# Performance work log

Measured on AMD Instinct MI355X. Metric: run time of the kernel, lower is better.

Reference implementation:

```python
import jax, jax.numpy as jnp
import numpy as np

DIM = 768
NUM_HEADS = 12
HEAD_DIM = DIM // NUM_HEADS
SCALE = HEAD_DIM ** -0.5


def setup_inputs() -> dict:
    key = jax.random.key(0)
    k1, k2, k3, k4 = jax.random.split(key, 4)
    B, N = 4, 2048
    x = jax.random.normal(k1, (B, N, DIM), dtype=jnp.float32)
    w_qkv = jax.random.normal(k2, (DIM, 3 * DIM), dtype=jnp.float32) * (DIM ** -0.5)
    w_proj = jax.random.normal(k3, (DIM, DIM), dtype=jnp.float32) * (DIM ** -0.5)
    b_proj = jax.random.normal(k4, (DIM,), dtype=jnp.float32) * 0.02
    return {"x": x, "w_qkv": w_qkv, "w_proj": w_proj, "b_proj": b_proj}


def reference(x, w_qkv, w_proj, b_proj):
    B, N, C = x.shape
    H, Dh = NUM_HEADS, HEAD_DIM
    # qkv: [B, N, 3, H, Dh] -> q,k,v each [B, H, N, Dh]
    qkv = (x @ w_qkv).reshape(B, N, 3, H, Dh)
    q = qkv[:, :, 0].transpose(0, 2, 1, 3) * SCALE
    k = qkv[:, :, 1].transpose(0, 2, 1, 3)
    v = qkv[:, :, 2].transpose(0, 2, 1, 3)
    attn = jax.nn.softmax(jnp.einsum('bhnd,bhmd->bhnm', q, k), axis=-1)
    out = jnp.einsum('bhnm,bhmd->bhnd', attn, v)  # [B, H, N, Dh]
    out = out.transpose(0, 2, 1, 3).reshape(B, N, C)
    return out @ w_proj + b_proj
```

## Files before the change

kernel.cpp:

```cpp
#include <hip/hip_runtime.h>

typedef unsigned short u16;
typedef __bf16 bf16x8 __attribute__((ext_vector_type(8)));
typedef __bf16 bf16x4 __attribute__((ext_vector_type(4)));
typedef short s16x4 __attribute__((ext_vector_type(4)));
typedef float f32x4 __attribute__((ext_vector_type(4)));
typedef unsigned short u16x8 __attribute__((ext_vector_type(8)));
typedef unsigned short u16x4 __attribute__((ext_vector_type(4)));

__device__ __forceinline__ u16 f2bf(float x) {
  union { float f; unsigned u; } c; c.f = x;
  unsigned r = c.u + 0x7FFFu + ((c.u >> 16) & 1u);
  return (u16)(r >> 16);
}

__device__ __forceinline__ void glds16(const void* g, void* s) {
  __builtin_amdgcn_global_load_lds(
      (const __attribute__((address_space(1))) unsigned int*)g,
      (__attribute__((address_space(3))) unsigned int*)s, 16, 0, 0);
}

__global__ __launch_bounds__(256) void k_cast_x(const float* __restrict__ x,
                                                u16* __restrict__ o) {
  int i = blockIdx.x * 256 + threadIdx.x;
  const f32x4* xp = (const f32x4*)x + (size_t)i * 2;
  f32x4 a = xp[0], b = xp[1];
  u16x8 r;
  r[0] = f2bf(a[0]); r[1] = f2bf(a[1]); r[2] = f2bf(a[2]); r[3] = f2bf(a[3]);
  r[4] = f2bf(b[0]); r[5] = f2bf(b[1]); r[6] = f2bf(b[2]); r[7] = f2bf(b[3]);
  *((u16x8*)o + i) = r;
}

__global__ __launch_bounds__(256) void k_transpose_w(const float* __restrict__ src,
                                                     u16* __restrict__ dst,
                                                     int K, int Nn) {
  __shared__ float tile[64 * 68];
  int tid = threadIdx.x;
  int n0 = blockIdx.x * 64, k0 = blockIdx.y * 64;
  int rr = tid >> 4, cc = tid & 15;
#pragma unroll
  for (int r = 0; r < 4; ++r) {
    int k = r * 16 + rr;
    f32x4 v = *(const f32x4*)(src + (size_t)(k0 + k) * Nn + n0 + cc * 4);
    *(f32x4*)(tile + k * 68 + cc * 4) = v;
  }
  __syncthreads();
#pragma unroll
  for (int r = 0; r < 4; ++r) {
    int n = r * 16 + rr;
    u16x4 o;
#pragma unroll
    for (int j = 0; j < 4; ++j) o[j] = f2bf(tile[(cc * 4 + j) * 68 + n]);
    *(u16x4*)(dst + (size_t)(n0 + n) * K + k0 + cc * 4) = o;
  }
}

template <int N, bool PROJ>
__global__ __launch_bounds__(256) void k_gemm(const u16* __restrict__ A,
                                              const u16* __restrict__ Bt,
                                              u16* __restrict__ Co,
                                              float* __restrict__ Cf,
                                              const float* __restrict__ bias) {
  const int K = 768;
  __shared__ u16 lA[128 * 64];
  __shared__ u16 lB[128 * 64];
  const int tid = threadIdx.x;
  const int wave = tid >> 6, lane = tid & 63;
  const int lr = lane & 15, lq = lane >> 4;
  const int m0 = blockIdx.x * 128, n0 = blockIdx.y * 128;
  const int wr = (wave >> 1) * 64, wc = (wave & 1) * 64;
  f32x4 acc[4][4] = {};
  for (int k0 = 0; k0 < K; k0 += 64) {
#pragma unroll
    for (int r = 0; r < 4; ++r) {
      int ch = r * 256 + tid;
      int mm = ch >> 3, cs = ch & 7;
      int k8 = (cs ^ (mm & 7)) << 3;
      glds16(A + (size_t)(m0 + mm) * K + k0 + k8, lA + ch * 8);
      glds16(Bt + (size_t)(n0 + mm) * K + k0 + k8, lB + ch * 8);
    }
    __syncthreads();
#pragma unroll
    for (int ks = 0; ks < 2; ++ks) {
      bf16x8 af[4], bfr[4];
#pragma unroll
      for (int f = 0; f < 4; ++f) {
        int ma = wr + f * 16 + lr;
        af[f] = *(const bf16x8*)(lA + (ma * 8 + ((ks * 4 + lq) ^ (ma & 7))) * 8);
        int nb = wc + f * 16 + lr;
        bfr[f] = *(const bf16x8*)(lB + (nb * 8 + ((ks * 4 + lq) ^ (nb & 7))) * 8);
      }
#pragma unroll
      for (int fi = 0; fi < 4; ++fi)
#pragma unroll
        for (int fj = 0; fj < 4; ++fj)
          acc[fi][fj] = __builtin_amdgcn_mfma_f32_16x16x32_bf16(
              af[fi], bfr[fj], acc[fi][fj], 0, 0, 0);
    }
    __syncthreads();
  }
#pragma unroll
  for (int fi = 0; fi < 4; ++fi) {
#pragma unroll
    for (int fj = 0; fj < 4; ++fj) {
      int row = m0 + wr + fi * 16 + lq * 4;
      int col = n0 + wc + fj * 16 + lr;
      if constexpr (PROJ) {
        float bv = bias[col];
#pragma unroll
        for (int g = 0; g < 4; ++g)
          Cf[(size_t)(row + g) * N + col] = acc[fi][fj][g] + bv;
      } else {
        const float qs = 0.18033688011112042f;
        float s = (col < 768) ? qs : 1.0f;
#pragma unroll
        for (int g = 0; g < 4; ++g)
          Co[(size_t)(row + g) * N + col] = f2bf(acc[fi][fj][g] * s);
      }
    }
  }
}

__global__ __launch_bounds__(256) void k_vtrans(const u16* __restrict__ qkv,
                                                u16* __restrict__ vt) {
  __shared__ u16 tile[64 * 72];
  int tid = threadIdx.x;
  int n0 = blockIdx.x * 64;
  int bh = blockIdx.y;
  int b = bh / 12, h = bh % 12;
  const u16* src = qkv + (size_t)(b * 2048 + n0) * 2304 + 1536 + h * 64;
#pragma unroll
  for (int r = 0; r < 2; ++r) {
    int n = r * 32 + (tid >> 3), c8 = tid & 7;
    u16x8 v = *(const u16x8*)(src + (size_t)n * 2304 + c8 * 8);
    *(u16x8*)(tile + n * 72 + c8 * 8) = v;
  }
  __syncthreads();
  u16* dstb = vt + (size_t)bh * 64 * 2048 + n0;
#pragma unroll
  for (int r = 0; r < 2; ++r) {
    int d = r * 32 + (tid >> 3), n8 = tid & 7;
    u16x8 o;
#pragma unroll
    for (int j = 0; j < 8; ++j) o[j] = tile[(n8 * 8 + j) * 72 + d];
    *(u16x8*)(dstb + (size_t)d * 2048 + n8 * 8) = o;
  }
}

__global__ __launch_bounds__(256) void k_attn(const u16* __restrict__ qkv,
                                              const u16* __restrict__ vt,
                                              u16* __restrict__ aout) {
  const int SEQ = 2048, C3 = 2304;
  __shared__ u16 lK[128 * 64];
  __shared__ u16 lV[64 * 128];
  const int tid = threadIdx.x;
  const int wave = tid >> 6, lane = tid & 63;
  const int lr = lane & 15, lq = lane >> 4;
  const int n0 = blockIdx.x * 128;
  const int bh = blockIdx.y;
  const int b = bh / 12, h = bh % 12;
  const u16* qb = qkv + (size_t)b * SEQ * C3 + h * 64;
  const u16* kb = qb + 768;
  const u16* vb = vt + (size_t)bh * 64 * SEQ;

#pragma unroll
  for (int r = 0; r < 4; ++r) {
    int ch = r * 256 + tid;
    int mm = ch >> 3, cs = ch & 7;
    glds16(qb + (size_t)(n0 + mm) * C3 + ((cs ^ (mm & 7)) << 3), lK + ch * 8);
  }
  __syncthreads();
  bf16x8 qf[2][2];
#pragma unroll
  for (int rf = 0; rf < 2; ++rf) {
    int mq = wave * 32 + rf * 16 + lr;
#pragma unroll
    for (int ks = 0; ks < 2; ++ks)
      qf[rf][ks] = *(const bf16x8*)(lK + (mq * 8 + ((ks * 4 + lq) ^ (mq & 7))) * 8);
  }

  f32x4 O[2][4] = {};
  float lsum[2] = {0.f, 0.f};

  for (int j0 = 0; j0 < SEQ; j0 += 128) {
    __syncthreads();
#pragma unroll
    for (int r = 0; r < 4; ++r) {
      int ch = r * 256 + tid;
      int mm = ch >> 3, cs = ch & 7;
      glds16(kb + (size_t)(j0 + mm) * C3 + ((cs ^ (mm & 7)) << 3), lK + ch * 8);
      int dd = ch >> 4, ct = ch & 15;
      glds16(vb + (size_t)dd * SEQ + j0 + ((ct ^ (dd & 7)) << 3), lV + ch * 8);
    }
    __syncthreads();

#pragma unroll
    for (int half = 0; half < 2; ++half) {
      f32x4 S[4][2];
#pragma unroll
      for (int cf = 0; cf < 4; ++cf)
#pragma unroll
        for (int rf = 0; rf < 2; ++rf)
          S[cf][rf] = (f32x4){-8.f, -8.f, -8.f, -8.f};
#pragma unroll
      for (int ks = 0; ks < 2; ++ks) {
#pragma unroll
        for (int cf = 0; cf < 4; ++cf) {
          int j = (half * 4 + cf) * 16 + lr;
          bf16x8 kf = *(const bf16x8*)(lK + (j * 8 + ((ks * 4 + lq) ^ (j & 7))) * 8);
#pragma unroll
          for (int rf = 0; rf < 2; ++rf)
            S[cf][rf] = __builtin_amdgcn_mfma_f32_16x16x32_bf16(
                kf, qf[rf][ks], S[cf][rf], 0, 0, 0);
        }
      }
      union PU { bf16x4 b; s16x4 s; } P[4][2];
#pragma unroll
      for (int cf = 0; cf < 4; ++cf)
#pragma unroll
        for (int rf = 0; rf < 2; ++rf) {
          f32x4 p;
#pragma unroll
          for (int g = 0; g < 4; ++g) p[g] = __builtin_amdgcn_exp2f(S[cf][rf][g]);
          lsum[rf] += (p[0] + p[1]) + (p[2] + p[3]);
          bf16x4 pb;
#pragma unroll
          for (int g = 0; g < 4; ++g) pb[g] = (__bf16)p[g];
          P[cf][rf].b = pb;
        }
#pragma unroll
      for (int cf = 0; cf < 4; ++cf) {
        int c2 = (half * 4 + cf) * 2 + (lq >> 1);
#pragma unroll
        for (int df = 0; df < 4; ++df) {
          int d = df * 16 + lr;
          s16x4 vf = *(const s16x4*)(lV + d * 128 + ((c2 ^ (d & 7)) << 3) + (lq & 1) * 4);
#pragma unroll
          for (int rf = 0; rf < 2; ++rf)
            O[rf][df] = __builtin_amdgcn_mfma_f32_16x16x16bf16_1k(
                vf, P[cf][rf].s, O[rf][df], 0, 0, 0);
        }
      }
    }
  }

#pragma unroll
  for (int rf = 0; rf < 2; ++rf) {
    float s = lsum[rf];
    s += __shfl_xor(s, 16);
    s += __shfl_xor(s, 32);
    float inv = 1.0f / s;
    int row = b * SEQ + n0 + wave * 32 + rf * 16 + lr;
#pragma unroll
    for (int df = 0; df < 4; ++df) {
      u16x4 o;
#pragma unroll
      for (int g = 0; g < 4; ++g) o[g] = f2bf(O[rf][df][g] * inv);
      *(u16x4*)(aout + (size_t)row * 768 + h * 64 + df * 16 + lq * 4) = o;
    }
  }
}

extern "C" void kernel_launch(void* const* d_in, const int* in_sizes, int n_in,
                              void* d_out, int out_size, void* d_ws, size_t ws_size,
                              hipStream_t stream) {
  const float* x = (const float*)d_in[0];
  const float* w_qkv = (const float*)d_in[1];
  const float* w_proj = (const float*)d_in[2];
  const float* b_proj = (const float*)d_in[3];
  float* out = (float*)d_out;
  char* ws = (char*)d_ws;
  u16* x_bf    = (u16*)(ws);
  u16* wqkv_t  = (u16*)(ws + 12582912);
  u16* wproj_t = (u16*)(ws + 16121856);
  u16* qkv     = (u16*)(ws + 17301504);
  u16* vt      = (u16*)(ws + 55050240);
  u16* aout    = (u16*)(ws + 67633152);

  k_cast_x<<<3072, 256, 0, stream>>>(x, x_bf);
  k_transpose_w<<<dim3(36, 12), 256, 0, stream>>>(w_qkv, wqkv_t, 768, 2304);
  k_transpose_w<<<dim3(12, 12), 256, 0, stream>>>(w_proj, wproj_t, 768, 768);
  k_gemm<2304, false><<<dim3(64, 18), 256, 0, stream>>>(x_bf, wqkv_t, qkv, nullptr, nullptr);
  k_vtrans<<<dim3(32, 48), 256, 0, stream>>>(qkv, vt);
  k_attn<<<dim3(16, 48), 256, 0, stream>>>(qkv, vt, aout);
  k_gemm<768, true><<<dim3(64, 6), 256, 0, stream>>>(aout, wproj_t, nullptr, out, b_proj);
}
```

Measured before the change: 247.4 us.

## Fuse V transpose into QKV GEMM and double-buffer attention K/V tiles

The QKV GEMM epilogue now writes the V columns straight into the transposed vt layout, which removes the separate k_vtrans kernel launch and its extra read and write of V. The attention kernel shrinks its query tile from 128 to 64 rows (doubling the grid) and uses 64-key tiles with two LDS buffers. The next K/V tile is prefetched with global_load_lds while the current one is computed, synchronised through manual s_waitcnt and s_barrier, with a launch-bounds occupancy hint of 5. The risks are scattered narrow stores in the GEMM epilogue and fragile hand-written wait counts.

```diff
diff --git a/kernel.cpp b/kernel.cpp
--- a/kernel.cpp
+++ b/kernel.cpp
@@ -60,7 +60,8 @@
                                               const u16* __restrict__ Bt,
                                               u16* __restrict__ Co,
                                               float* __restrict__ Cf,
-                                              const float* __restrict__ bias) {
+                                              const float* __restrict__ bias,
+                                              u16* __restrict__ vt) {
   const int K = 768;
   __shared__ u16 lA[128 * 64];
   __shared__ u16 lB[128 * 64];
@@ -111,52 +112,34 @@
         for (int g = 0; g < 4; ++g)
           Cf[(size_t)(row + g) * N + col] = acc[fi][fj][g] + bv;
       } else {
-        const float qs = 0.18033688011112042f;
-        float s = (col < 768) ? qs : 1.0f;
-#pragma unroll
-        for (int g = 0; g < 4; ++g)
-          Co[(size_t)(row + g) * N + col] = f2bf(acc[fi][fj][g] * s);
-      }
-    }
-  }
-}
-
-__global__ __launch_bounds__(256) void k_vtrans(const u16* __restrict__ qkv,
-                                                u16* __restrict__ vt) {
-  __shared__ u16 tile[64 * 72];
-  int tid = threadIdx.x;
-  int n0 = blockIdx.x * 64;
-  int bh = blockIdx.y;
-  int b = bh / 12, h = bh % 12;
-  const u16* src = qkv + (size_t)(b * 2048 + n0) * 2304 + 1536 + h * 64;
-#pragma unroll
-  for (int r = 0; r < 2; ++r) {
-    int n = r * 32 + (tid >> 3), c8 = tid & 7;
-    u16x8 v = *(const u16x8*)(src + (size_t)n * 2304 + c8 * 8);
-    *(u16x8*)(tile + n * 72 + c8 * 8) = v;
-  }
-  __syncthreads();
-  u16* dstb = vt + (size_t)bh * 64 * 2048 + n0;
-#pragma unroll
-  for (int r = 0; r < 2; ++r) {
-    int d = r * 32 + (tid >> 3), n8 = tid & 7;
-    u16x8 o;
-#pragma unroll
-    for (int j = 0; j < 8; ++j) o[j] = tile[(n8 * 8 + j) * 72 + d];
-    *(u16x8*)(dstb + (size_t)d * 2048 + n8 * 8) = o;
-  }
-}
-
-__global__ __launch_bounds__(256) void k_attn(const u16* __restrict__ qkv,
-                                              const u16* __restrict__ vt,
-                                              u16* __restrict__ aout) {
+        if (n0 + wc >= 1536) {
+          int hh = (col - 1536) >> 6, dd = col & 63;
+          u16x4 o;
+#pragma unroll
+          for (int g = 0; g < 4; ++g) o[g] = f2bf(acc[fi][fj][g]);
+          *(u16x4*)(vt + (((size_t)(row >> 11) * 12 + hh) * 64 + dd) * 2048 +
+                    (row & 2047)) = o;
+        } else {
+          const float qs = 0.18033688011112042f;
+          float s = (col < 768) ? qs : 1.0f;
+#pragma unroll
+          for (int g = 0; g < 4; ++g)
+            Co[(size_t)(row + g) * N + col] = f2bf(acc[fi][fj][g] * s);
+        }
+      }
+    }
+  }
+}
+
+__global__ __launch_bounds__(256, 5) void k_attn(const u16* __restrict__ qkv,
+                                                 const u16* __restrict__ vt,
+                                                 u16* __restrict__ aout) {
   const int SEQ = 2048, C3 = 2304;
-  __shared__ u16 lK[128 * 64];
-  __shared__ u16 lV[64 * 128];
+  __shared__ u16 lK0[64 * 64], lK1[64 * 64], lV0[64 * 64], lV1[64 * 64];
   const int tid = threadIdx.x;
   const int wave = tid >> 6, lane = tid & 63;
   const int lr = lane & 15, lq = lane >> 4;
-  const int n0 = blockIdx.x * 128;
+  const int n0 = blockIdx.x * 64;
   const int bh = blockIdx.y;
   const int b = bh / 12, h = bh % 12;
   const u16* qb = qkv + (size_t)b * SEQ * C3 + h * 64;
@@ -164,98 +147,101 @@
   const u16* vb = vt + (size_t)bh * 64 * SEQ;
 
 #pragma unroll
-  for (int r = 0; r < 4; ++r) {
+  for (int r = 0; r < 2; ++r) {
     int ch = r * 256 + tid;
     int mm = ch >> 3, cs = ch & 7;
-    glds16(qb + (size_t)(n0 + mm) * C3 + ((cs ^ (mm & 7)) << 3), lK + ch * 8);
+    glds16(qb + (size_t)(n0 + mm) * C3 + ((cs ^ (mm & 7)) << 3), lK0 + ch * 8);
   }
   __syncthreads();
-  bf16x8 qf[2][2];
-#pragma unroll
-  for (int rf = 0; rf < 2; ++rf) {
-    int mq = wave * 32 + rf * 16 + lr;
+  bf16x8 qf[2];
+  {
+    int mq = wave * 16 + lr;
 #pragma unroll
     for (int ks = 0; ks < 2; ++ks)
-      qf[rf][ks] = *(const bf16x8*)(lK + (mq * 8 + ((ks * 4 + lq) ^ (mq & 7))) * 8);
-  }
-
-  f32x4 O[2][4] = {};
-  float lsum[2] = {0.f, 0.f};
-
-  for (int j0 = 0; j0 < SEQ; j0 += 128) {
-    __syncthreads();
-#pragma unroll
-    for (int r = 0; r < 4; ++r) {
+      qf[ks] = *(const bf16x8*)(lK0 + (mq * 8 + ((ks * 4 + lq) ^ (mq & 7))) * 8);
+  }
+  __syncthreads();
+
+  f32x4 O[4] = {};
+  float lsum = 0.f;
+
+  auto stage = [&](int j0, u16* Kn, u16* Vn) {
+#pragma unroll
+    for (int r = 0; r < 2; ++r) {
       int ch = r * 256 + tid;
       int mm = ch >> 3, cs = ch & 7;
-      glds16(kb + (size_t)(j0 + mm) * C3 + ((cs ^ (mm & 7)) << 3), lK + ch * 8);
-      int dd = ch >> 4, ct = ch & 15;
-      glds16(vb + (size_t)dd * SEQ + j0 + ((ct ^ (dd & 7)) << 3), lV + ch * 8);
-    }
-    __syncthreads();
-
-#pragma unroll
-    for (int half = 0; half < 2; ++half) {
-      f32x4 S[4][2];
-#pragma unroll
-      for (int cf = 0; cf < 4; ++cf)
-#pragma unroll
-        for (int rf = 0; rf < 2; ++rf)
-          S[cf][rf] = (f32x4){-8.f, -8.f, -8.f, -8.f};
-#pragma unroll
-      for (int ks = 0; ks < 2; ++ks) {
-#pragma unroll
-        for (int cf = 0; cf < 4; ++cf) {
-          int j = (half * 4 + cf) * 16 + lr;
-          bf16x8 kf = *(const bf16x8*)(lK + (j * 8 + ((ks * 4 + lq) ^ (j & 7))) * 8);
-#pragma unroll
-          for (int rf = 0; rf < 2; ++rf)
-            S[cf][rf] = __builtin_amdgcn_mfma_f32_16x16x32_bf16(
-                kf, qf[rf][ks], S[cf][rf], 0, 0, 0);
-        }
-      }
-      union PU { bf16x4 b; s16x4 s; } P[4][2];
-#pragma unroll
-      for (int cf = 0; cf < 4; ++cf)
-#pragma unroll
-        for (int rf = 0; rf < 2; ++rf) {
-          f32x4 p;
-#pragma unroll
-          for (int g = 0; g < 4; ++g) p[g] = __builtin_amdgcn_exp2f(S[cf][rf][g]);
-          lsum[rf] += (p[0] + p[1]) + (p[2] + p[3]);
-          bf16x4 pb;
-#pragma unroll
-          for (int g = 0; g < 4; ++g) pb[g] = (__bf16)p[g];
-          P[cf][rf].b = pb;
-        }
+      glds16(kb + (size_t)(j0 + mm) * C3 + ((cs ^ (mm & 7)) << 3), Kn + ch * 8);
+    }
+#pragma unroll
+    for (int r = 0; r < 2; ++r) {
+      int ch = r * 256 + tid;
+      int dd = ch >> 3, ct = ch & 7;
+      glds16(vb + (size_t)dd * SEQ + j0 + ((ct ^ (dd & 7)) << 3), Vn + ch * 8);
+    }
+  };
+
+  auto do_iter = [&](int t, const u16* K_, const u16* V_, u16* Kn, u16* Vn) {
+    if (t < 31) {
+      stage((t + 1) * 64, Kn, Vn);
+      asm volatile("s_waitcnt vmcnt(4)" ::: "memory");
+    } else {
+      asm volatile("s_waitcnt vmcnt(0)" ::: "memory");
+    }
+    asm volatile("s_barrier" ::: "memory");
+    f32x4 S[4];
+#pragma unroll
+    for (int cf = 0; cf < 4; ++cf)
+      S[cf] = (f32x4){-8.f, -8.f, -8.f, -8.f};
+#pragma unroll
+    for (int ks = 0; ks < 2; ++ks)
 #pragma unroll
       for (int cf = 0; cf < 4; ++cf) {
-        int c2 = (half * 4 + cf) * 2 + (lq >> 1);
-#pragma unroll
-        for (int df = 0; df < 4; ++df) {
-          int d = df * 16 + lr;
-          s16x4 vf = *(const s16x4*)(lV + d * 128 + ((c2 ^ (d & 7)) << 3) + (lq & 1) * 4);
-#pragma unroll
-          for (int rf = 0; rf < 2; ++rf)
-            O[rf][df] = __builtin_amdgcn_mfma_f32_16x16x16bf16_1k(
-                vf, P[cf][rf].s, O[rf][df], 0, 0, 0);
-        }
-      }
-    }
-  }
-
-#pragma unroll
-  for (int rf = 0; rf < 2; ++rf) {
-    float s = lsum[rf];
+        int j = cf * 16 + lr;
+        bf16x8 kf = *(const bf16x8*)(K_ + (j * 8 + ((ks * 4 + lq) ^ (j & 7))) * 8);
+        S[cf] = __builtin_amdgcn_mfma_f32_16x16x32_bf16(kf, qf[ks], S[cf], 0, 0, 0);
+      }
+    union PU { bf16x4 b; s16x4 s; } P[4];
+#pragma unroll
+    for (int cf = 0; cf < 4; ++cf) {
+      f32x4 p;
+#pragma unroll
+      for (int g = 0; g < 4; ++g) p[g] = __builtin_amdgcn_exp2f(S[cf][g]);
+      lsum += (p[0] + p[1]) + (p[2] + p[3]);
+      bf16x4 pb;
+#pragma unroll
+      for (int g = 0; g < 4; ++g) pb[g] = (__bf16)p[g];
+      P[cf].b = pb;
+    }
+#pragma unroll
+    for (int cf = 0; cf < 4; ++cf) {
+      int c2 = cf * 2 + (lq >> 1);
+#pragma unroll
+      for (int df = 0; df < 4; ++df) {
+        int d = df * 16 + lr;
+        s16x4 vf = *(const s16x4*)(V_ + (d * 8 + (c2 ^ (d & 7))) * 8 + (lq & 1) * 4);
+        O[df] = __builtin_amdgcn_mfma_f32_16x16x16bf16_1k(vf, P[cf].s, O[df], 0, 0, 0);
+      }
+    }
+    asm volatile("s_barrier" ::: "memory");
+  };
+
+  stage(0, lK0, lV0);
+  for (int t = 0; t < 32; t += 2) {
+    do_iter(t, lK0, lV0, lK1, lV1);
+    do_iter(t + 1, lK1, lV1, lK0, lV0);
+  }
+
+  {
+    float s = lsum;
     s += __shfl_xor(s, 16);
     s += __shfl_xor(s, 32);
     float inv = 1.0f / s;
-    int row = b * SEQ + n0 + wave * 32 + rf * 16 + lr;
+    int row = b * SEQ + n0 + wave * 16 + lr;
 #pragma unroll
     for (int df = 0; df < 4; ++df) {
       u16x4 o;
 #pragma unroll
-      for (int g = 0; g < 4; ++g) o[g] = f2bf(O[rf][df][g] * inv);
+      for (int g = 0; g < 4; ++g) o[g] = f2bf(O[df][g] * inv);
       *(u16x4*)(aout + (size_t)row * 768 + h * 64 + df * 16 + lq * 4) = o;
     }
   }
@@ -280,8 +266,9 @@
   k_cast_x<<<3072, 256, 0, stream>>>(x, x_bf);
   k_transpose_w<<<dim3(36, 12), 256, 0, stream>>>(w_qkv, wqkv_t, 768, 2304);
   k_transpose_w<<<dim3(12, 12), 256, 0, stream>>>(w_proj, wproj_t, 768, 768);
-  k_gemm<2304, false><<<dim3(64, 18), 256, 0, stream>>>(x_bf, wqkv_t, qkv, nullptr, nullptr);
-  k_vtrans<<<dim3(32, 48), 256, 0, stream>>>(qkv, vt);
-  k_attn<<<dim3(16, 48), 256, 0, stream>>>(qkv, vt, aout);
-  k_gemm<768, true><<<dim3(64, 6), 256, 0, stream>>>(aout, wproj_t, nullptr, out, b_proj);
-}
+  k_gemm<2304, false><<<dim3(64, 18), 256, 0, stream>>>(x_bf, wqkv_t, qkv, nullptr,
+                                                        nullptr, vt);
+  k_attn<<<dim3(32, 48), 256, 0, stream>>>(qkv, vt, aout);
+  k_gemm<768, true><<<dim3(64, 6), 256, 0, stream>>>(aout, wproj_t, nullptr, out,
+                                                     b_proj, nullptr);
+}
```

After: 296.8 us. 1.2x slower.

## Split attention over key halves, fuse V transpose into QKV GEMM, shrink proj tile

Applied to the files above, without the earlier changes.

Attention now runs as a split-K (flash-decoding style) grid with two key halves per query tile. Each half writes unnormalized fp16 partial outputs and row sums, and a new merge kernel combines them and normalizes to bf16. This doubles the block count from 768 to 1536 to fill the GPU better. The separate V-transpose kernel is removed: the QKV GEMM epilogue writes V directly in transposed layout. The projection GEMM uses 64-row tiles for more blocks. Costs are an extra merge pass over the output, fp16 partials that could overflow or lose precision, and reuse of workspace buffers (x_bf, wqkv_t) after they are consumed.

```diff
diff --git a/kernel.cpp b/kernel.cpp
--- a/kernel.cpp
+++ b/kernel.cpp
@@ -5,6 +5,7 @@
 typedef __bf16 bf16x4 __attribute__((ext_vector_type(4)));
 typedef short s16x4 __attribute__((ext_vector_type(4)));
 typedef float f32x4 __attribute__((ext_vector_type(4)));
+typedef _Float16 f16x4 __attribute__((ext_vector_type(4)));
 typedef unsigned short u16x8 __attribute__((ext_vector_type(8)));
 typedef unsigned short u16x4 __attribute__((ext_vector_type(4)));
 
@@ -55,43 +56,52 @@
   }
 }
 
-template <int N, bool PROJ>
+template <int BM, int N, bool PROJ>
 __global__ __launch_bounds__(256) void k_gemm(const u16* __restrict__ A,
                                               const u16* __restrict__ Bt,
                                               u16* __restrict__ Co,
                                               float* __restrict__ Cf,
-                                              const float* __restrict__ bias) {
+                                              const float* __restrict__ bias,
+                                              u16* __restrict__ vt) {
   const int K = 768;
-  __shared__ u16 lA[128 * 64];
+  const int FI = BM / 32;
+  __shared__ u16 lA[BM * 64];
   __shared__ u16 lB[128 * 64];
   const int tid = threadIdx.x;
   const int wave = tid >> 6, lane = tid & 63;
   const int lr = lane & 15, lq = lane >> 4;
-  const int m0 = blockIdx.x * 128, n0 = blockIdx.y * 128;
-  const int wr = (wave >> 1) * 64, wc = (wave & 1) * 64;
-  f32x4 acc[4][4] = {};
+  const int m0 = blockIdx.x * BM, n0 = blockIdx.y * 128;
+  const int wr = (wave >> 1) * (BM / 2), wc = (wave & 1) * 64;
+  f32x4 acc[FI][4] = {};
   for (int k0 = 0; k0 < K; k0 += 64) {
+#pragma unroll
+    for (int r = 0; r < BM / 32; ++r) {
+      int ch = r * 256 + tid;
+      int mm = ch >> 3, cs = ch & 7;
+      glds16(A + (size_t)(m0 + mm) * K + k0 + ((cs ^ (mm & 7)) << 3), lA + ch * 8);
+    }
 #pragma unroll
     for (int r = 0; r < 4; ++r) {
       int ch = r * 256 + tid;
       int mm = ch >> 3, cs = ch & 7;
-      int k8 = (cs ^ (mm & 7)) << 3;
-      glds16(A + (size_t)(m0 + mm) * K + k0 + k8, lA + ch * 8);
-      glds16(Bt + (size_t)(n0 + mm) * K + k0 + k8, lB + ch * 8);
+      glds16(Bt + (size_t)(n0 + mm) * K + k0 + ((cs ^ (mm & 7)) << 3), lB + ch * 8);
     }
     __syncthreads();
 #pragma unroll
     for (int ks = 0; ks < 2; ++ks) {
-      bf16x8 af[4], bfr[4];
-#pragma unroll
-      for (int f = 0; f < 4; ++f) {
+      bf16x8 af[FI], bfr[4];
+#pragma unroll
+      for (int f = 0; f < FI; ++f) {
         int ma = wr + f * 16 + lr;
         af[f] = *(const bf16x8*)(lA + (ma * 8 + ((ks * 4 + lq) ^ (ma & 7))) * 8);
+      }
+#pragma unroll
+      for (int f = 0; f < 4; ++f) {
         int nb = wc + f * 16 + lr;
         bfr[f] = *(const bf16x8*)(lB + (nb * 8 + ((ks * 4 + lq) ^ (nb & 7))) * 8);
       }
 #pragma unroll
-      for (int fi = 0; fi < 4; ++fi)
+      for (int fi = 0; fi < FI; ++fi)
 #pragma unroll
         for (int fj = 0; fj < 4; ++fj)
           acc[fi][fj] = __builtin_amdgcn_mfma_f32_16x16x32_bf16(
@@ -100,7 +110,7 @@
     __syncthreads();
   }
 #pragma unroll
-  for (int fi = 0; fi < 4; ++fi) {
+  for (int fi = 0; fi < FI; ++fi) {
 #pragma unroll
     for (int fj = 0; fj < 4; ++fj) {
       int row = m0 + wr + fi * 16 + lq * 4;
@@ -111,45 +121,30 @@
         for (int g = 0; g < 4; ++g)
           Cf[(size_t)(row + g) * N + col] = acc[fi][fj][g] + bv;
       } else {
-        const float qs = 0.18033688011112042f;
-        float s = (col < 768) ? qs : 1.0f;
-#pragma unroll
-        for (int g = 0; g < 4; ++g)
-          Co[(size_t)(row + g) * N + col] = f2bf(acc[fi][fj][g] * s);
-      }
-    }
-  }
-}
-
-__global__ __launch_bounds__(256) void k_vtrans(const u16* __restrict__ qkv,
-                                                u16* __restrict__ vt) {
-  __shared__ u16 tile[64 * 72];
-  int tid = threadIdx.x;
-  int n0 = blockIdx.x * 64;
-  int bh = blockIdx.y;
-  int b = bh / 12, h = bh % 12;
-  const u16* src = qkv + (size_t)(b * 2048 + n0) * 2304 + 1536 + h * 64;
-#pragma unroll
-  for (int r = 0; r < 2; ++r) {
-    int n = r * 32 + (tid >> 3), c8 = tid & 7;
-    u16x8 v = *(const u16x8*)(src + (size_t)n * 2304 + c8 * 8);
-    *(u16x8*)(tile + n * 72 + c8 * 8) = v;
-  }
-  __syncthreads();
-  u16* dstb = vt + (size_t)bh * 64 * 2048 + n0;
-#pragma unroll
-  for (int r = 0; r < 2; ++r) {
-    int d = r * 32 + (tid >> 3), n8 = tid & 7;
-    u16x8 o;
-#pragma unroll
-    for (int j = 0; j < 8; ++j) o[j] = tile[(n8 * 8 + j) * 72 + d];
-    *(u16x8*)(dstb + (size_t)d * 2048 + n8 * 8) = o;
+        if (n0 + wc >= 1536) {
+          int hh = (col - 1536) >> 6, dd = col & 63;
+          u16x4 o;
+#pragma unroll
+          for (int g = 0; g < 4; ++g) o[g] = f2bf(acc[fi][fj][g]);
+          *(u16x4*)(vt + (((size_t)(row >> 11) * 12 + hh) * 64 + dd) * 2048 +
+                    (row & 2047)) = o;
+        } else {
+          const float qs = 0.18033688011112042f;
+          float s = (col < 768) ? qs : 1.0f;
+#pragma unroll
+          for (int g = 0; g < 4; ++g)
+            Co[(size_t)(row + g) * N + col] = f2bf(acc[fi][fj][g] * s);
+        }
+      }
+    }
   }
 }
 
 __global__ __launch_bounds__(256) void k_attn(const u16* __restrict__ qkv,
                                               const u16* __restrict__ vt,
-                                              u16* __restrict__ aout) {
+                                              u16* __restrict__ p0,
+                                              u16* __restrict__ p1,
+                                              float* __restrict__ Lp) {
   const int SEQ = 2048, C3 = 2304;
   __shared__ u16 lK[128 * 64];
   __shared__ u16 lV[64 * 128];
@@ -158,6 +153,7 @@
   const int lr = lane & 15, lq = lane >> 4;
   const int n0 = blockIdx.x * 128;
   const int bh = blockIdx.y;
+  const int jh = blockIdx.z;
   const int b = bh / 12, h = bh % 12;
   const u16* qb = qkv + (size_t)b * SEQ * C3 + h * 64;
   const u16* kb = qb + 768;
@@ -182,7 +178,8 @@
   f32x4 O[2][4] = {};
   float lsum[2] = {0.f, 0.f};
 
-  for (int j0 = 0; j0 < SEQ; j0 += 128) {
+  for (int tt = 0; tt < 8; ++tt) {
+    int j0 = jh * 1024 + tt * 128;
     __syncthreads();
 #pragma unroll
     for (int r = 0; r < 4; ++r) {
@@ -244,21 +241,44 @@
     }
   }
 
+  u16* pd = jh ? p1 : p0;
+  float* Lb = Lp + (size_t)(jh * 48 + bh) * 2048;
 #pragma unroll
   for (int rf = 0; rf < 2; ++rf) {
     float s = lsum[rf];
     s += __shfl_xor(s, 16);
     s += __shfl_xor(s, 32);
-    float inv = 1.0f / s;
-    int row = b * SEQ + n0 + wave * 32 + rf * 16 + lr;
+    int rowl = n0 + wave * 32 + rf * 16 + lr;
+    if (lq == 0) Lb[rowl] = s;
+    size_t row = (size_t)b * SEQ + rowl;
 #pragma unroll
     for (int df = 0; df < 4; ++df) {
-      u16x4 o;
-#pragma unroll
-      for (int g = 0; g < 4; ++g) o[g] = f2bf(O[rf][df][g] * inv);
-      *(u16x4*)(aout + (size_t)row * 768 + h * 64 + df * 16 + lq * 4) = o;
-    }
-  }
+      union { f16x4 h; u16x4 u; } o;
+#pragma unroll
+      for (int g = 0; g < 4; ++g) o.h[g] = (_Float16)O[rf][df][g];
+      *(u16x4*)(pd + row * 768 + h * 64 + df * 16 + lq * 4) = o.u;
+    }
+  }
+}
+
+__global__ __launch_bounds__(256) void k_merge(const u16* __restrict__ p0,
+                                               u16* __restrict__ p1,
+                                               const float* __restrict__ Lp) {
+  int t = blockIdx.x * 256 + threadIdx.x;
+  int row = t / 192, c4 = (t % 192) * 4;
+  int hh = c4 >> 6;
+  int bh = (row >> 11) * 12 + hh, rowl = row & 2047;
+  float l = Lp[(size_t)bh * 2048 + rowl] + Lp[(size_t)(48 + bh) * 2048 + rowl];
+  float inv = 1.0f / l;
+  size_t off = (size_t)row * 768 + c4;
+  union { f16x4 h; u16x4 u; } a, bb;
+  a.u = *(const u16x4*)(p0 + off);
+  bb.u = *(const u16x4*)(p1 + off);
+  u16x4 o;
+#pragma unroll
+  for (int g = 0; g < 4; ++g)
+    o[g] = f2bf(((float)a.h[g] + (float)bb.h[g]) * inv);
+  *(u16x4*)(p1 + off) = o;
 }
 
 extern "C" void kernel_launch(void* const* d_in, const int* in_sizes, int n_in,
@@ -276,12 +296,15 @@
   u16* qkv     = (u16*)(ws + 17301504);
   u16* vt      = (u16*)(ws + 55050240);
   u16* aout    = (u16*)(ws + 67633152);
+  float* Lp    = (float*)wqkv_t;
 
   k_cast_x<<<3072, 256, 0, stream>>>(x, x_bf);
   k_transpose_w<<<dim3(36, 12), 256, 0, stream>>>(w_qkv, wqkv_t, 768, 2304);
   k_transpose_w<<<dim3(12, 12), 256, 0, stream>>>(w_proj, wproj_t, 768, 768);
-  k_gemm<2304, false><<<dim3(64, 18), 256, 0, stream>>>(x_bf, wqkv_t, qkv, nullptr, nullptr);
-  k_vtrans<<<dim3(32, 48), 256, 0, stream>>>(qkv, vt);
-  k_attn<<<dim3(16, 48), 256, 0, stream>>>(qkv, vt, aout);
-  k_gemm<768, true><<<dim3(64, 6), 256, 0, stream>>>(aout, wproj_t, nullptr, out, b_proj);
-}
+  k_gemm<128, 2304, false><<<dim3(64, 18), 256, 0, stream>>>(x_bf, wqkv_t, qkv,
+                                                             nullptr, nullptr, vt);
+  k_attn<<<dim3(16, 48, 2), 256, 0, stream>>>(qkv, vt, x_bf, aout, Lp);
+  k_merge<<<6144, 256, 0, stream>>>(x_bf, aout, Lp);
+  k_gemm<64, 768, true><<<dim3(128, 6), 256, 0, stream>>>(aout, wproj_t, nullptr,
+                                                          out, b_proj, nullptr);
+}
```

Result: faster. 241.2 us (-2.5%).
